# Performance work log

Hardware: AMD Instinct MI355X
Metric: run time of the kernel (lower is better)

The kernel has to match this reference:

```python
import jax, jax.numpy as jnp
import numpy as np

PATCH = 8
EPS = 1e-5


def setup_inputs() -> dict:
    key = jax.random.key(0)
    k0, k1, k2 = jax.random.split(key, 3)
    B, C, H, W = 8, 256, 256, 256
    r = 8
    x = jax.random.normal(k0, (B, C, H, W), dtype=jnp.float32)
    gamma = jnp.ones((C,), dtype=jnp.float32)   # LayerNorm weight
    beta = jnp.zeros((C,), dtype=jnp.float32)   # LayerNorm bias
    # torch Linear weights: [out, in], bias=False
    w1 = jax.random.normal(k1, (C // r, C), dtype=jnp.float32) * (1.0 / np.sqrt(C))
    w2 = jax.random.normal(k2, (C, C // r), dtype=jnp.float32) * (1.0 / np.sqrt(C // r))
    return {"x": x, "gamma": gamma, "beta": beta, "w1": w1, "w2": w2}


def reference(x, gamma, beta, w1, w2):
    # x: [B, C, H, W]; H, W divisible by PATCH (no-pad path of the module)
    B, C, H, W = x.shape
    ph = pw = PATCH
    nH, nW = H // ph, W // pw

    # LayerNorm over channel dim (module permutes patches to channel-last before norm;
    # per-pixel channel LN is invariant to the patch regrouping)
    xcl = jnp.transpose(x, (0, 2, 3, 1))                    # [B, H, W, C]
    mu = jnp.mean(xcl, axis=-1, keepdims=True)
    var = jnp.mean(jnp.square(xcl - mu), axis=-1, keepdims=True)
    xn = (xcl - mu) * jax.lax.rsqrt(var + EPS) * gamma + beta

    # patchify: [B, nH, ph, nW, pw, C]
    xp = xn.reshape(B, nH, ph, nW, pw, C)

    # per-patch, per-channel mean of the normalized tensor -> [B, nH, nW, C]
    pm = jnp.mean(xp, axis=(2, 4))

    # SE-style gating MLP (Linear no bias -> SiLU -> Linear no bias -> sigmoid)
    h = jax.nn.silu(jnp.einsum('bijc,rc->bijr', pm, w1))    # [B, nH, nW, C//r]
    gate = jax.nn.sigmoid(jnp.einsum('bijr,cr->bijc', h, w2))  # [B, nH, nW, C]

    # scale normalized patches by per-patch channel gates and scatter back
    out = xp * gate[:, :, None, :, None, :]                 # [B, nH, ph, nW, pw, C]
    out = out.reshape(B, H, W, C)
    return jnp.transpose(out, (0, 3, 1, 2))                 # [B, C, H, W]
```

## Files before the change

kernel.cpp:

```cpp
#include <hip/hip_runtime.h>
#include <hip/hip_bf16.h>
#include <math.h>

#define C_DIM 256
#define HWDIM 256
#define CH_STRIDE (HWDIM * HWDIM)
#define R_DIM 32
#define PXW 130

typedef float nfloat4 __attribute__((ext_vector_type(4)));

__global__
void lpa_fused_kernel(const float* __restrict__ x,
                      const float* __restrict__ gamma,
                      const float* __restrict__ beta,
                      const float* __restrict__ w1,
                      const float* __restrict__ w2,
                      float* __restrict__ out)
{
    __shared__ __hip_bfloat162 xl[C_DIM * PXW];
    __shared__ float sp1[256];
    __shared__ float sq1[256];
    __shared__ float mu_s[256];
    __shared__ float rs_s[256];
    __shared__ float gs[C_DIM];
    __shared__ float bs[C_DIM];
    __shared__ float pm_s[4 * C_DIM];
    __shared__ float h_s[4 * R_DIM];
    __shared__ float2 AB_s[4 * C_DIM];

    const int t    = threadIdx.x;
    const int wid  = t >> 6;
    const int lane = t & 63;
    const int hh   = lane >> 3;
    const int wq   = lane & 7;
    const int pat  = wq >> 1;
    const int p0   = hh * 32 + wq * 4;
    const int p2   = p0 >> 1;

    if (t < 256) { sp1[t] = 0.f; sq1[t] = 0.f; gs[t] = gamma[t]; bs[t] = beta[t]; }
    __syncthreads();

    const int bid = blockIdx.x;
    const int b   = bid >> 8;
    const int ij  = bid & 255;
    const unsigned H0 = (unsigned)(ij >> 3) * 8u;
    const unsigned W0 = (unsigned)(ij & 7) * 32u;
    const unsigned rowoff = (unsigned)b * (C_DIM * CH_STRIDE)
                          + (H0 + (unsigned)hh) * HWDIM + W0 + (unsigned)wq * 4u;
    const float* xb = x + rowoff + (unsigned)wid * 16u * CH_STRIDE;

    float s0 = 0.f, s1 = 0.f, s2 = 0.f, s3 = 0.f;
    float q0 = 0.f, q1 = 0.f, q2 = 0.f, q3 = 0.f;
#pragma unroll
    for (int k = 0; k < 16; ++k) {
        float4 f = *reinterpret_cast<const float4*>(xb + (unsigned)k * CH_STRIDE);
        s0 += f.x; q0 += f.x * f.x;
        s1 += f.y; q1 += f.y * f.y;
        s2 += f.z; q2 += f.z * f.z;
        s3 += f.w; q3 += f.w * f.w;
        __hip_bfloat162 lo = __float22bfloat162_rn(make_float2(f.x, f.y));
        __hip_bfloat162 hi = __float22bfloat162_rn(make_float2(f.z, f.w));
        uint2 wv;
        wv.x = *reinterpret_cast<const unsigned*>(&lo);
        wv.y = *reinterpret_cast<const unsigned*>(&hi);
        const int c = wid * 16 + k;
        *reinterpret_cast<uint2*>(&xl[c * PXW + p2]) = wv;
    }
    atomicAdd(&sp1[p0 + 0], s0); atomicAdd(&sq1[p0 + 0], q0);
    atomicAdd(&sp1[p0 + 1], s1); atomicAdd(&sq1[p0 + 1], q1);
    atomicAdd(&sp1[p0 + 2], s2); atomicAdd(&sq1[p0 + 2], q2);
    atomicAdd(&sp1[p0 + 3], s3); atomicAdd(&sq1[p0 + 3], q3);
    __syncthreads();

    if (t < 256) {
        float mu  = sp1[t] * (1.0f / 256.0f);
        float var = sq1[t] * (1.0f / 256.0f) - mu * mu;
        mu_s[t] = mu;
        rs_s[t] = rsqrtf(var + 1e-5f);
    }
    __syncthreads();

    {
        const int c  = t & 255;
        const int pt = t >> 8;
        const __hip_bfloat162* row = &xl[c * PXW];
        float acc = 0.f;
#pragma unroll
        for (int h2 = 0; h2 < 8; ++h2) {
            const int pbase = h2 * 32 + pt * 8;
            const int wbase = (pbase >> 1);
#pragma unroll
            for (int j = 0; j < 4; ++j) {
                float2 xy = __bfloat1622float2(row[wbase + j]);
                const int p = pbase + j * 2;
                acc += rs_s[p]     * (xy.x - mu_s[p])
                     + rs_s[p + 1] * (xy.y - mu_s[p + 1]);
            }
        }
        pm_s[pt * C_DIM + c] = gs[c] * acc * (1.0f / 64.0f) + bs[c];
    }
    __syncthreads();

    {
        const int pat4 = t >> 8;
        const int r    = (t >> 3) & 31;
        const int k8   = t & 7;
        const float4* wrow = reinterpret_cast<const float4*>(w1 + r * C_DIM + k8 * 32);
        const float* pmk = &pm_s[pat4 * C_DIM + k8 * 32];
        float s = 0.f;
#pragma unroll
        for (int j = 0; j < 8; ++j) {
            float4 wv = wrow[j];
            float4 pv = *reinterpret_cast<const float4*>(pmk + j * 4);
            s += wv.x * pv.x + wv.y * pv.y + wv.z * pv.z + wv.w * pv.w;
        }
        s += __shfl_down(s, 4, 8);
        s += __shfl_down(s, 2, 8);
        s += __shfl_down(s, 1, 8);
        if (k8 == 0) {
            float sig = 1.0f / (1.0f + __expf(-s));
            h_s[pat4 * R_DIM + r] = s * sig;
        }
    }
    __syncthreads();

    {
        const int pat4 = t >> 8;
        const int c4   = t & 255;
        const float4* wrow = reinterpret_cast<const float4*>(w2 + c4 * R_DIM);
        const float* hk = &h_s[pat4 * R_DIM];
        float s = 0.f;
#pragma unroll
        for (int j = 0; j < 8; ++j) {
            float4 wv = wrow[j];
            s += wv.x * hk[j * 4 + 0] + wv.y * hk[j * 4 + 1]
               + wv.z * hk[j * 4 + 2] + wv.w * hk[j * 4 + 3];
        }
        float gate = 1.0f / (1.0f + __expf(-s));
        AB_s[pat4 * C_DIM + c4] = make_float2(gs[c4] * gate, bs[c4] * gate);
    }
    __syncthreads();

    {
        const float4 mu4 = *reinterpret_cast<const float4*>(&mu_s[p0]);
        const float4 rs4 = *reinterpret_cast<const float4*>(&rs_s[p0]);
        float* ob = out + rowoff + (unsigned)wid * 16u * CH_STRIDE;
#pragma unroll
        for (int k = 0; k < 16; ++k) {
            const int c = wid * 16 + k;
            float2 ab = AB_s[pat * C_DIM + c];
            uint2 wv = *reinterpret_cast<const uint2*>(&xl[c * PXW + p2]);
            __hip_bfloat162 lo = *reinterpret_cast<const __hip_bfloat162*>(&wv.x);
            __hip_bfloat162 hi = *reinterpret_cast<const __hip_bfloat162*>(&wv.y);
            float2 xy = __bfloat1622float2(lo);
            float2 zw = __bfloat1622float2(hi);
            nfloat4 o;
            o.x = ab.x * rs4.x * (xy.x - mu4.x) + ab.y;
            o.y = ab.x * rs4.y * (xy.y - mu4.y) + ab.y;
            o.z = ab.x * rs4.z * (zw.x - mu4.z) + ab.y;
            o.w = ab.x * rs4.w * (zw.y - mu4.w) + ab.y;
            __builtin_nontemporal_store(o,
                reinterpret_cast<nfloat4*>(ob + (unsigned)k * CH_STRIDE));
        }
    }
}

extern "C" void kernel_launch(void* const* d_in, const int* in_sizes, int n_in,
                              void* d_out, int out_size, void* d_ws, size_t ws_size,
                              hipStream_t stream) {
    const float* x     = (const float*)d_in[0];
    const float* gamma = (const float*)d_in[1];
    const float* beta  = (const float*)d_in[2];
    const float* w1    = (const float*)d_in[3];
    const float* w2    = (const float*)d_in[4];
    float* out = (float*)d_out;

    const int B = in_sizes[0] / (C_DIM * HWDIM * HWDIM);
    const int nwg = B * 256;

    lpa_fused_kernel<<<nwg, 1024, 0, stream>>>(x, gamma, beta, w1, w2, out);
}
```

Before: 272.5 us.

## Halve per-block tile to two patches, remap XCD block order, use plain stores

Each workgroup now covers an 8x16 pixel region (two patches) with 512 threads instead of 8x32 with 1024, which halves the LDS tile and doubles the grid so more workgroups can be resident per CU. The channel mapping changes to interleaved channels (c0 + 16k), and each wavefront splits into two half-waves over channels. Block IDs are remapped so consecutive logical tiles land on the same XCD, and the nontemporal output stores become ordinary stores. The trade-off is that each 64-byte row segment is now read as only 16 contiguous floats per row, and the gating MLP weights are reloaded for twice as many blocks.

```diff
diff --git a/kernel.cpp b/kernel.cpp
--- a/kernel.cpp
+++ b/kernel.cpp
@@ -6,9 +6,7 @@
 #define HWDIM 256
 #define CH_STRIDE (HWDIM * HWDIM)
 #define R_DIM 32
-#define PXW 130
-
-typedef float nfloat4 __attribute__((ext_vector_type(4)));
+#define XPITCH 65
 
 __global__
 void lpa_fused_kernel(const float* __restrict__ x,
@@ -16,45 +14,53 @@
                       const float* __restrict__ beta,
                       const float* __restrict__ w1,
                       const float* __restrict__ w2,
-                      float* __restrict__ out)
+                      float* __restrict__ out,
+                      int nwg)
 {
-    __shared__ __hip_bfloat162 xl[C_DIM * PXW];
-    __shared__ float sp1[256];
-    __shared__ float sq1[256];
-    __shared__ float mu_s[256];
-    __shared__ float rs_s[256];
+    __shared__ __hip_bfloat162 xl[C_DIM * XPITCH];
+    __shared__ float sp1[128];
+    __shared__ float sq1[128];
+    __shared__ float mu_s[128];
+    __shared__ float rs_s[128];
     __shared__ float gs[C_DIM];
     __shared__ float bs[C_DIM];
-    __shared__ float pm_s[4 * C_DIM];
-    __shared__ float h_s[4 * R_DIM];
-    __shared__ float2 AB_s[4 * C_DIM];
+    __shared__ float pm_s[2 * C_DIM];
+    __shared__ float h_s[2 * R_DIM];
+    __shared__ float2 AB_s[2 * C_DIM];
 
     const int t    = threadIdx.x;
     const int wid  = t >> 6;
     const int lane = t & 63;
-    const int hh   = lane >> 3;
-    const int wq   = lane & 7;
-    const int pat  = wq >> 1;
-    const int p0   = hh * 32 + wq * 4;
-    const int p2   = p0 >> 1;
+    const int par  = lane >> 5;
+    const int pos  = lane & 31;
+    const int row  = pos >> 2;
+    const int qc   = pos & 3;
+    const int pat  = qc >> 1;
+    const int p0   = row * 16 + qc * 4;
+    const int p2w  = (p0 >> 1);
 
-    if (t < 256) { sp1[t] = 0.f; sq1[t] = 0.f; gs[t] = gamma[t]; bs[t] = beta[t]; }
+    if (t < 128) { sp1[t] = 0.f; sq1[t] = 0.f; }
+    if (t < C_DIM) { gs[t] = gamma[t]; bs[t] = beta[t]; }
     __syncthreads();
 
     const int bid = blockIdx.x;
-    const int b   = bid >> 8;
-    const int ij  = bid & 255;
-    const unsigned H0 = (unsigned)(ij >> 3) * 8u;
-    const unsigned W0 = (unsigned)(ij & 7) * 32u;
+    const int per_xcd = nwg >> 3;
+    const int pid = (bid & 7) * per_xcd + (bid >> 3);
+
+    const int b  = pid >> 9;
+    const int ij = pid & 511;
+    const unsigned H0 = (unsigned)(ij >> 4) * 8u;
+    const unsigned W0 = (unsigned)(ij & 15) * 16u;
     const unsigned rowoff = (unsigned)b * (C_DIM * CH_STRIDE)
-                          + (H0 + (unsigned)hh) * HWDIM + W0 + (unsigned)wq * 4u;
-    const float* xb = x + rowoff + (unsigned)wid * 16u * CH_STRIDE;
+                          + (H0 + (unsigned)row) * HWDIM + W0 + (unsigned)qc * 4u;
+    const unsigned c0 = (unsigned)wid * 2u + (unsigned)par;
+    const float* xb = x + rowoff + c0 * CH_STRIDE;
 
     float s0 = 0.f, s1 = 0.f, s2 = 0.f, s3 = 0.f;
     float q0 = 0.f, q1 = 0.f, q2 = 0.f, q3 = 0.f;
 #pragma unroll
     for (int k = 0; k < 16; ++k) {
-        float4 f = *reinterpret_cast<const float4*>(xb + (unsigned)k * CH_STRIDE);
+        float4 f = *reinterpret_cast<const float4*>(xb + (unsigned)(k * 16) * CH_STRIDE);
         s0 += f.x; q0 += f.x * f.x;
         s1 += f.y; q1 += f.y * f.y;
         s2 += f.z; q2 += f.z * f.z;
@@ -64,8 +70,8 @@
         uint2 wv;
         wv.x = *reinterpret_cast<const unsigned*>(&lo);
         wv.y = *reinterpret_cast<const unsigned*>(&hi);
-        const int c = wid * 16 + k;
-        *reinterpret_cast<uint2*>(&xl[c * PXW + p2]) = wv;
+        const int c = (int)c0 + k * 16;
+        *reinterpret_cast<uint2*>(&xl[c * XPITCH + p2w]) = wv;
     }
     atomicAdd(&sp1[p0 + 0], s0); atomicAdd(&sq1[p0 + 0], q0);
     atomicAdd(&sp1[p0 + 1], s1); atomicAdd(&sq1[p0 + 1], q1);
@@ -73,7 +79,7 @@
     atomicAdd(&sp1[p0 + 3], s3); atomicAdd(&sq1[p0 + 3], q3);
     __syncthreads();
 
-    if (t < 256) {
+    if (t < 128) {
         float mu  = sp1[t] * (1.0f / 256.0f);
         float var = sq1[t] * (1.0f / 256.0f) - mu * mu;
         mu_s[t] = mu;
@@ -84,15 +90,15 @@
     {
         const int c  = t & 255;
         const int pt = t >> 8;
-        const __hip_bfloat162* row = &xl[c * PXW];
+        const __hip_bfloat162* crow = &xl[c * XPITCH + pt * 4];
         float acc = 0.f;
 #pragma unroll
-        for (int h2 = 0; h2 < 8; ++h2) {
-            const int pbase = h2 * 32 + pt * 8;
-            const int wbase = (pbase >> 1);
+        for (int r8 = 0; r8 < 8; ++r8) {
+            const int wbase = r8 * 8;
+            const int pbase = r8 * 16 + pt * 8;
 #pragma unroll
             for (int j = 0; j < 4; ++j) {
-                float2 xy = __bfloat1622float2(row[wbase + j]);
+                float2 xy = __bfloat1622float2(crow[wbase + j]);
                 const int p = pbase + j * 2;
                 acc += rs_s[p]     * (xy.x - mu_s[p])
                      + rs_s[p + 1] * (xy.y - mu_s[p + 1]);
@@ -103,11 +109,11 @@
     __syncthreads();
 
     {
-        const int pat4 = t >> 8;
-        const int r    = (t >> 3) & 31;
-        const int k8   = t & 7;
+        const int pt = t >> 8;
+        const int r  = (t >> 3) & 31;
+        const int k8 = t & 7;
         const float4* wrow = reinterpret_cast<const float4*>(w1 + r * C_DIM + k8 * 32);
-        const float* pmk = &pm_s[pat4 * C_DIM + k8 * 32];
+        const float* pmk = &pm_s[pt * C_DIM + k8 * 32];
         float s = 0.f;
 #pragma unroll
         for (int j = 0; j < 8; ++j) {
@@ -120,16 +126,16 @@
         s += __shfl_down(s, 1, 8);
         if (k8 == 0) {
             float sig = 1.0f / (1.0f + __expf(-s));
-            h_s[pat4 * R_DIM + r] = s * sig;
+            h_s[pt * R_DIM + r] = s * sig;
         }
     }
     __syncthreads();
 
     {
-        const int pat4 = t >> 8;
-        const int c4   = t & 255;
+        const int pt = t >> 8;
+        const int c4 = t & 255;
         const float4* wrow = reinterpret_cast<const float4*>(w2 + c4 * R_DIM);
-        const float* hk = &h_s[pat4 * R_DIM];
+        const float* hk = &h_s[pt * R_DIM];
         float s = 0.f;
 #pragma unroll
         for (int j = 0; j < 8; ++j) {
@@ -138,30 +144,29 @@
                + wv.z * hk[j * 4 + 2] + wv.w * hk[j * 4 + 3];
         }
         float gate = 1.0f / (1.0f + __expf(-s));
-        AB_s[pat4 * C_DIM + c4] = make_float2(gs[c4] * gate, bs[c4] * gate);
+        AB_s[pt * C_DIM + c4] = make_float2(gs[c4] * gate, bs[c4] * gate);
     }
     __syncthreads();
 
     {
         const float4 mu4 = *reinterpret_cast<const float4*>(&mu_s[p0]);
         const float4 rs4 = *reinterpret_cast<const float4*>(&rs_s[p0]);
-        float* ob = out + rowoff + (unsigned)wid * 16u * CH_STRIDE;
+        float* ob = out + rowoff + c0 * CH_STRIDE;
 #pragma unroll
         for (int k = 0; k < 16; ++k) {
-            const int c = wid * 16 + k;
+            const int c = (int)c0 + k * 16;
             float2 ab = AB_s[pat * C_DIM + c];
-            uint2 wv = *reinterpret_cast<const uint2*>(&xl[c * PXW + p2]);
+            uint2 wv = *reinterpret_cast<const uint2*>(&xl[c * XPITCH + p2w]);
             __hip_bfloat162 lo = *reinterpret_cast<const __hip_bfloat162*>(&wv.x);
             __hip_bfloat162 hi = *reinterpret_cast<const __hip_bfloat162*>(&wv.y);
             float2 xy = __bfloat1622float2(lo);
             float2 zw = __bfloat1622float2(hi);
-            nfloat4 o;
+            float4 o;
             o.x = ab.x * rs4.x * (xy.x - mu4.x) + ab.y;
             o.y = ab.x * rs4.y * (xy.y - mu4.y) + ab.y;
             o.z = ab.x * rs4.z * (zw.x - mu4.z) + ab.y;
             o.w = ab.x * rs4.w * (zw.y - mu4.w) + ab.y;
-            __builtin_nontemporal_store(o,
-                reinterpret_cast<nfloat4*>(ob + (unsigned)k * CH_STRIDE));
+            *reinterpret_cast<float4*>(ob + (unsigned)(k * 16) * CH_STRIDE) = o;
         }
     }
 }
@@ -177,7 +182,7 @@
     float* out = (float*)d_out;
 
     const int B = in_sizes[0] / (C_DIM * HWDIM * HWDIM);
-    const int nwg = B * 256;
+    const int nwg = B * 512;
 
-    lpa_fused_kernel<<<nwg, 1024, 0, stream>>>(x, gamma, beta, w1, w2, out);
+    lpa_fused_kernel<<<nwg, 512, 0, stream>>>(x, gamma, beta, w1, w2, out, nwg);
 }
```

After: 288.9 us. 1.06x slower.
